# Kernel optimization log

Hardware: AMD Instinct MI355X
Metric: run time of the kernel (lower is better)

## Reference

```python
import jax, jax.numpy as jnp
import numpy as np

B, D = 128, 16384
EPS = 0.05
MAX_DEPTH = 5
D_MAX = 1000.0


def setup_inputs() -> dict:
    key = jax.random.key(0)
    k1, k2 = jax.random.split(key)
    theta = jax.random.normal(k1, (B, D), dtype=jnp.float32)
    prec = jax.random.uniform(k2, (D,), dtype=jnp.float32)
    return {"theta": theta, "prec": prec}


def _energy(theta, prec):
    # per-chain potential energy U(theta): [B]
    return 0.5 * jnp.einsum('bd,d,bd->b', theta, prec, theta)


def _grad_energy(theta, prec):
    # mirrors torch autograd.grad(energy.sum(), theta)
    return jax.grad(lambda th: _energy(th, prec).sum())(theta)


def _bdot(a, b):
    return jnp.einsum('bd,bd->b', a, b)


def _leapfrog(theta, r, prec, eps):
    gU = _grad_energy(theta, prec)
    r = r - 0.5 * eps * gU
    theta = theta + eps * r
    e = _energy(theta, prec)
    gU = _grad_energy(theta, prec)
    r = r - 0.5 * eps * gU
    return theta, r, e


def _buildtree(theta, r, u, eps_dir, j, key, prec):
    # returns (theta_near, r_near, theta_far, r_far, theta_prop, n, s)
    if j == 0:
        th, rp, e = _leapfrog(theta, r, prec, eps_dir)
        H = e + 0.5 * _bdot(rp, rp)
        n_p = (u <= jnp.exp(-H)).astype(jnp.int32)
        s_p = (jnp.log(u) - D_MAX < -H).astype(jnp.int32)
        return th, rp, th, rp, th, n_p, s_p
    k1, k2, k3 = jax.random.split(key, 3)
    th_n, r_n, th_f, r_f, th_p, n_p, s_p = _buildtree(theta, r, u, eps_dir, j - 1, k1, prec)
    _, _, th_f2, r_f2, th_pp, n_pp, s_pp = _buildtree(th_f, r_f, u, eps_dir, j - 1, k2, prec)
    # accept proposal from second subtree with prob n'' / (n' + n''), masked by s'
    denom = jnp.maximum(n_p + n_pp, 1).astype(jnp.float32)
    flag = (jax.random.uniform(k3, n_p.shape) < n_pp.astype(jnp.float32) / denom) & (s_p >= 1)
    th_p = jnp.where(flag[:, None], th_pp, th_p)
    # u-turn check; v*(far - near) == theta_plus - theta_minus
    v = jnp.sign(eps_dir)
    d = th_f2 - th_n
    s_new = (s_p * s_pp
             * ((v * _bdot(d, r_n)) >= 0.0).astype(jnp.int32)
             * ((v * _bdot(d, r_f2)) >= 0.0).astype(jnp.int32))
    n_new = n_p + jnp.where(s_p >= 1, n_pp, 0)
    return th_n, r_n, th_f2, r_f2, th_p, n_new, s_new


def _sample_trajectory(theta0, prec, key):
    kr, ku, key = jax.random.split(key, 3)
    r0 = jax.random.normal(kr, theta0.shape, theta0.dtype)
    H0 = _energy(theta0, prec) + 0.5 * _bdot(r0, r0)
    u = jax.random.uniform(ku, H0.shape, theta0.dtype) * jnp.exp(-H0)
    theta_r = theta0
    theta_f = theta0
    r_r = r0
    r_f = r0
    theta_m = theta0
    n = jnp.ones((theta0.shape[0],), jnp.int32)
    s = jnp.ones((theta0.shape[0],), jnp.int32)
    for j in range(MAX_DEPTH):  # tree doubling, bounded depth (jit-friendly)
        key, kv, kt, ka = jax.random.split(key, 4)
        v = jnp.where(jax.random.normal(kv, ()) >= 0.0, 1.0, -1.0)
        neg = v < 0.0
        st_th = jnp.where(neg, theta_r, theta_f)
        st_r = jnp.where(neg, r_r, r_f)
        _, _, th_far, r_far, th_p, n_p, s_p = _buildtree(st_th, st_r, u, v * EPS, j, kt, prec)
        theta_r = jnp.where(neg, th_far, theta_r)
        r_r = jnp.where(neg, r_far, r_r)
        theta_f = jnp.where(neg, theta_f, th_far)
        r_f = jnp.where(neg, r_f, r_far)
        acc = jax.random.uniform(ka, n.shape) < jnp.minimum(
            n_p.astype(jnp.float32) / n.astype(jnp.float32), 1.0)
        acc = acc & (s >= 1) & (s_p >= 1)
        theta_m = jnp.where(acc[:, None], th_p, theta_m)
        n = n + jnp.where(s >= 1, n_p, 0)
        d = theta_f - theta_r
        s = (s * s_p
             * (_bdot(d, r_r) >= 0.0).astype(jnp.int32)
             * (_bdot(d, r_f) >= 0.0).astype(jnp.int32))
    return theta_m


def reference(theta, prec):
    return _sample_trajectory(theta, prec, jax.random.key(42))
```

## Files before the change

### kernel.cpp

```cpp
#include <hip/hip_runtime.h>
#include <cstdint>
#include <cstring>


#define PARTITIONABLE 1

constexpr int NCHAIN = 128;
constexpr int NDIM   = 16384;
constexpr int VD     = 4;
constexpr int TPB    = 256;
constexpr int WGPC   = NDIM / (TPB * VD);
constexpr int NW     = NDIM / (64 * VD);
constexpr int NSLOT  = 62;
constexpr int NNODE  = 26;
constexpr float EPS  = 0.05f;

static_assert(NDIM % (TPB * VD) == 0, "tiling");

__host__ __device__ static inline void tf2(uint32_t k0, uint32_t k1,
                                           uint32_t x0, uint32_t x1,
                                           uint32_t& o0, uint32_t& o1) {
  const uint32_t ks2 = k0 ^ k1 ^ 0x1BD11BDAu;
  x0 += k0; x1 += k1;
#define TF_R(r) { x0 += x1; x1 = (x1 << (r)) | (x1 >> (32 - (r))); x1 ^= x0; }
  TF_R(13) TF_R(15) TF_R(26) TF_R(6)
  x0 += k1;  x1 += ks2 + 1u;
  TF_R(17) TF_R(29) TF_R(16) TF_R(24)
  x0 += ks2; x1 += k0 + 2u;
  TF_R(13) TF_R(15) TF_R(26) TF_R(6)
  x0 += k0;  x1 += k1 + 3u;
  TF_R(17) TF_R(29) TF_R(16) TF_R(24)
  x0 += k1;  x1 += ks2 + 4u;
  TF_R(13) TF_R(15) TF_R(26) TF_R(6)
  x0 += ks2; x1 += k0 + 5u;
#undef TF_R
  o0 = x0; o1 = x1;
}

__device__ static inline float u01(uint32_t bits) {
  return __uint_as_float((bits >> 9) | 0x3f800000u) - 1.0f;
}

__device__ static inline float erfinv32(float x) {
  float w = -log1pf(-x * x);
  float p;
  if (w < 5.0f) {
    w -= 2.5f;
    p = 2.81022636e-08f;
    p = fmaf(p, w, 3.43273939e-07f);
    p = fmaf(p, w, -3.5233877e-06f);
    p = fmaf(p, w, -4.39150654e-06f);
    p = fmaf(p, w, 0.00021858087f);
    p = fmaf(p, w, -0.00125372503f);
    p = fmaf(p, w, -0.00417768164f);
    p = fmaf(p, w, 0.246640727f);
    p = fmaf(p, w, 1.50140941f);
  } else {
    w = sqrtf(w) - 3.0f;
    p = -0.000200214257f;
    p = fmaf(p, w, 0.000100950558f);
    p = fmaf(p, w, 0.00134934322f);
    p = fmaf(p, w, -0.00367342844f);
    p = fmaf(p, w, 0.00573950773f);
    p = fmaf(p, w, -0.0076224613f);
    p = fmaf(p, w, 0.00943887047f);
    p = fmaf(p, w, 1.00167406f);
    p = fmaf(p, w, 2.83297682f);
  }
  return p * x;
}

__device__ static inline float norm_from_bits(uint32_t bits) {
  const float lo = __uint_as_float(0xBF7FFFFFu);
  float u = fmaxf(lo, fmaf(u01(bits), 2.0f, lo));
  return __uint_as_float(0x3FB504F3u) * erfinv32(u);
}

__device__ static inline float r0_elem(uint32_t k0, uint32_t k1, uint32_t i) {
#if PARTITIONABLE
  uint32_t a, c; tf2(k0, k1, 0u, i, a, c);
  return norm_from_bits(a ^ c);
#else
  const uint32_t H = (uint32_t)(NCHAIN * NDIM / 2);
  uint32_t a, c;
  if (i < H) { tf2(k0, k1, i, i + H, a, c); return norm_from_bits(a); }
  else       { tf2(k0, k1, i - H, i, a, c); return norm_from_bits(c); }
#endif
}

__device__ static inline float unif_chain(uint32_t k0, uint32_t k1, int b) {
#if PARTITIONABLE
  uint32_t a, c; tf2(k0, k1, 0u, (uint32_t)b, a, c);
  return u01(a ^ c);
#else
  uint32_t a, c;
  if (b < 64) { tf2(k0, k1, (uint32_t)b, (uint32_t)(b + 64), a, c); return u01(a); }
  else        { tf2(k0, k1, (uint32_t)(b - 64), (uint32_t)b, a, c); return u01(c); }
#endif
}

#define DPP_ADD(x, ctrl, rm)                                                   \
  (x) += __int_as_float(__builtin_amdgcn_update_dpp(                           \
      0, __float_as_int(x), (ctrl), (rm), 0xf, true));

__device__ static inline float wave_sum63(float x) {
  DPP_ADD(x, 0x111, 0xf)
  DPP_ADD(x, 0x112, 0xf)
  DPP_ADD(x, 0x114, 0xf)
  DPP_ADD(x, 0x118, 0xf)
  DPP_ADD(x, 0x142, 0xa)
  DPP_ADD(x, 0x143, 0xc)
  return x;
}

struct TrajParams { int v[5]; };
struct K2Params {
  uint32_t nk0[NNODE], nk1[NNODE];
  uint32_t ak0[5], ak1[5];
  int v[5];
};

struct St {
  float tha[VD], ra[VD], tho[VD], ro[VD], pc[VD];
  float nt[5][VD], nr[5][VD];
};

template <int J, int I>
__device__ __forceinline__ void leaf_body(St& st, const float e, const float he,
                                          float* __restrict__ partials,
                                          const int chain, const int wv,
                                          const int lane, int& slot) {
#pragma unroll
  for (int d = 0; d < VD; ++d) {
    st.ra[d]  = fmaf(-he, st.pc[d] * st.tha[d], st.ra[d]);
    st.tha[d] = fmaf(e, st.ra[d], st.tha[d]);
    st.ra[d]  = fmaf(-he, st.pc[d] * st.tha[d], st.ra[d]);
  }
  constexpr int P = __builtin_popcount((unsigned)I);
#pragma unroll
  for (int d = 0; d < VD; ++d) { st.nt[P][d] = st.tha[d]; st.nr[P][d] = st.ra[d]; }
  constexpr int M = __builtin_ctz(~(unsigned)I);
#pragma unroll
  for (int k = 0; k < M; ++k) {
    const int s1 = P - 1 - k;
    float d1 = 0.f, d2 = 0.f;
#pragma unroll
    for (int d = 0; d < VD; ++d) {
      float dd = st.tha[d] - st.nt[s1][d];
      d1 = fmaf(dd, st.nr[s1][d], d1);
      d2 = fmaf(dd, st.ra[d], d2);
    }
    d1 = wave_sum63(d1);
    d2 = wave_sum63(d2);
    if (lane == 63) {
      partials[((size_t)(slot    ) * NCHAIN + chain) * NW + wv] = d1;
      partials[((size_t)(slot + 1) * NCHAIN + chain) * NW + wv] = d2;
    }
    slot += 2;
  }
}

template <int J, int I>
__device__ __forceinline__ void run_level(St& st, const float e, const float he,
                                          float* __restrict__ partials,
                                          const int chain, const int wv,
                                          const int lane, int& slot) {
  leaf_body<J, I>(st, e, he, partials, chain, wv, lane, slot);
  if constexpr (I + 1 < (1 << J))
    run_level<J, I + 1>(st, e, he, partials, chain, wv, lane, slot);
}

__launch_bounds__(TPB, 2)
__global__ void k_traj0(const float* __restrict__ th0g, const float* __restrict__ precg,
                        uint32_t kr0, uint32_t kr1,
                        float* __restrict__ partials, TrajParams P) {
  const int tid     = threadIdx.x;
  const int chain   = blockIdx.x / WGPC;
  const int sblk    = blockIdx.x % WGPC;
  const int dimBase = sblk * (TPB * VD) + tid * VD;
  const int lane    = tid & 63;
  const int wv      = sblk * (TPB / 64) + (tid >> 6);
  const uint32_t flat = (uint32_t)chain * NDIM + dimBase;

  St st;
  {
    const float4 t = *reinterpret_cast<const float4*>(th0g + (size_t)chain * NDIM + dimBase);
    const float4 p = *reinterpret_cast<const float4*>(precg + dimBase);
    st.tha[0]=t.x; st.tha[1]=t.y; st.tha[2]=t.z; st.tha[3]=t.w;
    st.pc [0]=p.x; st.pc [1]=p.y; st.pc [2]=p.z; st.pc [3]=p.w;
  }
#pragma unroll
  for (int d = 0; d < VD; ++d) st.ra[d] = r0_elem(kr0, kr1, flat + (uint32_t)d);
#pragma unroll
  for (int d = 0; d < VD; ++d) { st.tho[d] = st.tha[d]; st.ro[d] = st.ra[d]; }

  int slot = 0;
  bool cur_fwd = true;

#define LEVEL(J)                                                               \
  {                                                                            \
    const bool fwd = P.v[J] > 0;                                               \
    if (fwd != cur_fwd) {                                                      \
      _Pragma("unroll")                                                        \
      for (int d = 0; d < VD; ++d) {                                           \
        float t;                                                               \
        t = st.tha[d]; st.tha[d] = st.tho[d]; st.tho[d] = t;                   \
        t = st.ra[d];  st.ra[d]  = st.ro[d];  st.ro[d]  = t;                   \
      }                                                                        \
    }                                                                          \
    cur_fwd = fwd;                                                             \
    const float e  = fwd ? EPS : -EPS;                                         \
    const float he = 0.5f * e;                                                 \
    run_level<J, 0>(st, e, he, partials, chain, wv, lane, slot);               \
    float p1 = 0.f, p2 = 0.f;                                                  \
    _Pragma("unroll")                                                          \
    for (int d = 0; d < VD; ++d) {                                             \
      float dd = st.tha[d] - st.tho[d];                                        \
      p1 = fmaf(dd, st.ra[d], p1);                                             \
      p2 = fmaf(dd, st.ro[d], p2);                                             \
    }                                                                          \
    p1 = wave_sum63(p1);                                                       \
    p2 = wave_sum63(p2);                                                       \
    if (lane == 63) {                                                          \
      partials[((size_t)(slot    ) * NCHAIN + chain) * NW + wv] = p1;          \
      partials[((size_t)(slot + 1) * NCHAIN + chain) * NW + wv] = p2;          \
    }                                                                          \
    slot += 2;                                                                 \
  }

  LEVEL(0) LEVEL(1) LEVEL(2) LEVEL(3) LEVEL(4)
#undef LEVEL
}

__global__ void k_red(const float* __restrict__ partials, float* __restrict__ dots) {
  int gid  = blockIdx.x * blockDim.x + threadIdx.x;
  int w    = gid >> 6;
  int lane = gid & 63;
  if (w >= NSLOT * NCHAIN) return;
  float v = partials[(size_t)w * NW + lane];
  v = wave_sum63(v);
  if (lane == 63) dots[w] = v;
}

__global__ void k_logic(const float* __restrict__ dots, int* __restrict__ selg,
                        K2Params P) {
  int b = threadIdx.x;
  if (b >= NCHAIN) return;
  int n = 1, s = 1, sel = -1;
  int slot = 0, nodeidx = 0, g = 0;
  int st_n[6], st_s[6], st_p[6];
  for (int j = 0; j < 5; ++j) {
    float vj = (P.v[j] > 0) ? 1.0f : -1.0f;
    int sp = 0;
    int NL = 1 << j;
    for (int i = 0; i < NL; ++i) {
      st_n[sp] = 1; st_s[sp] = 1; st_p[sp] = g; sp++; g++;
      int m = __builtin_ctz(~(unsigned)i);
      for (int k = 0; k < m; ++k) {
        int n1 = st_n[sp-2], s1 = st_s[sp-2], p1i = st_p[sp-2];
        int n2 = st_n[sp-1], s2 = st_s[sp-1], p2i = st_p[sp-1];
        float d1 = dots[(size_t)(slot    ) * NCHAIN + b];
        float d2 = dots[(size_t)(slot + 1) * NCHAIN + b];
        slot += 2;
        float uu = unif_chain(P.nk0[nodeidx], P.nk1[nodeidx], b);
        nodeidx++;
        int   dn    = n1 + n2; if (dn < 1) dn = 1;
        bool  flag  = (uu < (float)n2 / (float)dn) && (s1 >= 1);
        int   pm    = flag ? p2i : p1i;
        int   sm    = (s1 != 0 && s2 != 0 &&
                       (vj * d1 >= 0.0f) && (vj * d2 >= 0.0f)) ? 1 : 0;
        int   nm    = n1 + ((s1 >= 1) ? n2 : 0);
        st_n[sp-2] = nm; st_s[sp-2] = sm; st_p[sp-2] = pm;
        sp--;
      }
    }
    int n_p = st_n[0], s_p = st_s[0], th_p = st_p[0];
    float q1 = dots[(size_t)(slot    ) * NCHAIN + b];
    float q2 = dots[(size_t)(slot + 1) * NCHAIN + b];
    slot += 2;
    float dm1, dm2;
    if (P.v[j] > 0) { dm1 = q2;  dm2 = q1; }
    else            { dm1 = -q1; dm2 = -q2; }
    float au = unif_chain(P.ak0[j], P.ak1[j], b);
    float ratio = fminf((float)n_p / (float)n, 1.0f);
    bool acc = (au < ratio) && (s >= 1) && (s_p >= 1);
    if (acc) sel = th_p;
    n = n + ((s >= 1) ? n_p : 0);
    s = (s != 0 && s_p != 0 && (dm1 >= 0.0f) && (dm2 >= 0.0f)) ? 1 : 0;
  }
  selg[b] = sel;
}

__launch_bounds__(TPB, 2)
__global__ void k_gather(const float* __restrict__ th0g, const float* __restrict__ precg,
                         uint32_t kr0, uint32_t kr1,
                         const int* __restrict__ selg, float* __restrict__ outg,
                         TrajParams P) {
  const int chain   = blockIdx.x / WGPC;
  const int sblk    = blockIdx.x % WGPC;
  const int dimBase = sblk * (TPB * VD) + threadIdx.x * VD;
  const uint32_t flat = (uint32_t)chain * NDIM + dimBase;
  const int sel = selg[chain];

  float tha[VD], ra[VD], tho[VD], ro[VD], pc[VD], outv[VD];
  {
    const float4 t = *reinterpret_cast<const float4*>(th0g + (size_t)chain * NDIM + dimBase);
    const float4 p = *reinterpret_cast<const float4*>(precg + dimBase);
    tha[0]=t.x; tha[1]=t.y; tha[2]=t.z; tha[3]=t.w;
    pc [0]=p.x; pc [1]=p.y; pc [2]=p.z; pc [3]=p.w;
  }
#pragma unroll
  for (int d = 0; d < VD; ++d) outv[d] = tha[d];
  if (sel >= 0) {
#pragma unroll
    for (int d = 0; d < VD; ++d) ra[d] = r0_elem(kr0, kr1, flat + (uint32_t)d);
#pragma unroll
    for (int d = 0; d < VD; ++d) { tho[d] = tha[d]; ro[d] = ra[d]; }
    int g = 0;
    bool cur_fwd = true;
    bool done = false;
    for (int j = 0; j < 5 && !done; ++j) {
      const bool fwd = P.v[j] > 0;
      if (fwd != cur_fwd) {
#pragma unroll
        for (int d = 0; d < VD; ++d) {
          float t;
          t = tha[d]; tha[d] = tho[d]; tho[d] = t;
          t = ra[d];  ra[d]  = ro[d];  ro[d]  = t;
        }
      }
      cur_fwd = fwd;
      const float e  = fwd ? EPS : -EPS;
      const float he = 0.5f * e;
      const int NL = 1 << j;
      for (int i = 0; i < NL; ++i) {
#pragma unroll
        for (int d = 0; d < VD; ++d) {
          ra[d]  = fmaf(-he, pc[d] * tha[d], ra[d]);
          tha[d] = fmaf(e, ra[d], tha[d]);
          ra[d]  = fmaf(-he, pc[d] * tha[d], ra[d]);
        }
        if (g == sel) {
#pragma unroll
          for (int d = 0; d < VD; ++d) outv[d] = tha[d];
          done = true;
          break;
        }
        g++;
      }
    }
  }
  float4 o; o.x = outv[0]; o.y = outv[1]; o.z = outv[2]; o.w = outv[3];
  *reinterpret_cast<float4*>(outg + (size_t)chain * NDIM + dimBase) = o;
}

static inline float host_bits_to_f(uint32_t fb) { float f; std::memcpy(&f, &fb, 4); return f; }

static void host_split(uint32_t k0, uint32_t k1, int nsub, uint32_t* o0, uint32_t* o1) {
#if PARTITIONABLE
  for (int i = 0; i < nsub; ++i) tf2(k0, k1, 0u, (uint32_t)i, o0[i], o1[i]);
#else
  uint32_t A[8], C[8], flat[16];
  for (int i = 0; i < nsub; ++i) tf2(k0, k1, (uint32_t)i, (uint32_t)(nsub + i), A[i], C[i]);
  for (int i = 0; i < nsub; ++i) { flat[i] = A[i]; flat[nsub + i] = C[i]; }
  for (int j = 0; j < nsub; ++j) { o0[j] = flat[2*j]; o1[j] = flat[2*j + 1]; }
#endif
}

static int host_vsign(uint32_t k0, uint32_t k1) {
  uint32_t a, c; tf2(k0, k1, 0u, 0u, a, c);
#if PARTITIONABLE
  uint32_t bits = a ^ c;
#else
  uint32_t bits = a;
#endif
  float f  = host_bits_to_f((bits >> 9) | 0x3f800000u) - 1.0f;
  float lo = host_bits_to_f(0xBF7FFFFFu);
  float u  = f * 2.0f + lo;
  return (u >= 0.0f) ? 1 : -1;
}

static void gen_nodes(uint32_t k0, uint32_t k1, int j,
                      uint32_t* nk0, uint32_t* nk1, int& idx) {
  if (j == 0) return;
  uint32_t o0[3], o1[3];
  host_split(k0, k1, 3, o0, o1);
  gen_nodes(o0[0], o1[0], j - 1, nk0, nk1, idx);
  gen_nodes(o0[1], o1[1], j - 1, nk0, nk1, idx);
  nk0[idx] = o0[2]; nk1[idx] = o1[2]; idx++;
}

extern "C" void kernel_launch(void* const* d_in, const int* in_sizes, int n_in,
                              void* d_out, int out_size, void* d_ws, size_t ws_size,
                              hipStream_t stream) {
  const float* th0  = (const float*)d_in[0];
  const float* prec = (const float*)d_in[1];
  float* out = (float*)d_out;

  float* partials = (float*)d_ws;
  float* dots     = partials + (size_t)NSLOT * NCHAIN * NW;
  int*   sel      = (int*)(dots + (size_t)NSLOT * NCHAIN);

  uint32_t key0 = 0u, key1 = 42u;
  uint32_t s0[4], s1[4];
  host_split(key0, key1, 3, s0, s1);
  const uint32_t kr0 = s0[0], kr1 = s1[0];
  key0 = s0[2]; key1 = s1[2];

  K2Params P2; TrajParams PT;
  int idx = 0;
  for (int j = 0; j < 5; ++j) {
    host_split(key0, key1, 4, s0, s1);
    key0 = s0[0]; key1 = s1[0];
    int v = host_vsign(s0[1], s1[1]);
    P2.v[j] = v; PT.v[j] = v;
    gen_nodes(s0[2], s1[2], j, P2.nk0, P2.nk1, idx);
    P2.ak0[j] = s0[3]; P2.ak1[j] = s1[3];
  }

  k_traj0<<<dim3(NCHAIN * WGPC), dim3(TPB), 0, stream>>>(
      th0, prec, kr0, kr1, partials, PT);
  k_red<<<dim3((NSLOT * NCHAIN * 64) / TPB), dim3(TPB), 0, stream>>>(partials, dots);
  k_logic<<<dim3(1), dim3(NCHAIN), 0, stream>>>(dots, sel, P2);
  k_gather<<<dim3(NCHAIN * WGPC), dim3(TPB), 0, stream>>>(
      th0, prec, kr0, kr1, sel, out, PT);
}
```

Measured before the change: 123.6 us.

## Fuse trajectory, reduction, NUTS logic and gather into one last-block kernel

```diff
diff --git a/kernel.cpp b/kernel.cpp
--- a/kernel.cpp
+++ b/kernel.cpp
@@ -113,8 +113,7 @@
   return x;
 }
 
-struct TrajParams { int v[5]; };
-struct K2Params {
+struct Params {
   uint32_t nk0[NNODE], nk1[NNODE];
   uint32_t ak0[5], ak1[5];
   int v[5];
@@ -170,10 +169,73 @@
     run_level<J, I + 1>(st, e, he, partials, chain, wv, lane, slot);
 }
 
+struct SM {
+  int n, s, sel, slot, nodeidx, g;
+  int st_n[5], st_s[5], st_p[5];
+};
+
+template <int J, int I>
+__device__ __forceinline__ void sm_leaf(SM& m, const float* dots_s,
+                                        const float* unifs_s, const float vj) {
+  constexpr int P = __builtin_popcount((unsigned)I);
+  m.st_n[P] = 1; m.st_s[P] = 1; m.st_p[P] = m.g; m.g++;
+  constexpr int M = __builtin_ctz(~(unsigned)I);
+#pragma unroll
+  for (int k = 0; k < M; ++k) {
+    const int t = P - k;
+    int n1 = m.st_n[t-1], s1 = m.st_s[t-1], p1 = m.st_p[t-1];
+    int n2 = m.st_n[t],   s2 = m.st_s[t],   p2 = m.st_p[t];
+    float d1 = dots_s[m.slot], d2 = dots_s[m.slot + 1];
+    m.slot += 2;
+    float uu = unifs_s[m.nodeidx]; m.nodeidx++;
+    int dn = n1 + n2; if (dn < 1) dn = 1;
+    bool fl = (uu < (float)n2 / (float)dn) && (s1 >= 1);
+    m.st_p[t-1] = fl ? p2 : p1;
+    m.st_s[t-1] = (s1 != 0 && s2 != 0 &&
+                   (vj * d1 >= 0.0f) && (vj * d2 >= 0.0f)) ? 1 : 0;
+    m.st_n[t-1] = n1 + ((s1 >= 1) ? n2 : 0);
+  }
+}
+
+template <int J, int I>
+__device__ __forceinline__ void sm_level(SM& m, const float* dots_s,
+                                         const float* unifs_s, const float vj) {
+  sm_leaf<J, I>(m, dots_s, unifs_s, vj);
+  if constexpr (I + 1 < (1 << J))
+    sm_level<J, I + 1>(m, dots_s, unifs_s, vj);
+}
+
+template <int J>
+__device__ __forceinline__ void sm_close(SM& m, const float* dots_s,
+                                         const float* unifs_s, const int vj) {
+  int n_p = m.st_n[0], s_p = m.st_s[0], th_p = m.st_p[0];
+  float q1 = dots_s[m.slot], q2 = dots_s[m.slot + 1];
+  m.slot += 2;
+  float dm1, dm2;
+  if (vj > 0) { dm1 = q2;  dm2 = q1; }
+  else        { dm1 = -q1; dm2 = -q2; }
+  float au = unifs_s[NNODE + J];
+  float ratio = fminf((float)n_p / (float)m.n, 1.0f);
+  bool acc = (au < ratio) && (m.s >= 1) && (s_p >= 1);
+  if (acc) m.sel = th_p;
+  m.n = m.n + ((m.s >= 1) ? n_p : 0);
+  m.s = (m.s != 0 && s_p != 0 && (dm1 >= 0.0f) && (dm2 >= 0.0f)) ? 1 : 0;
+}
+
+__global__ void k_zero(unsigned* __restrict__ done) {
+  if (threadIdx.x < NCHAIN) done[threadIdx.x] = 0u;
+}
+
 __launch_bounds__(TPB, 2)
-__global__ void k_traj0(const float* __restrict__ th0g, const float* __restrict__ precg,
-                        uint32_t kr0, uint32_t kr1,
-                        float* __restrict__ partials, TrajParams P) {
+__global__ void k_main(const float* __restrict__ th0g, const float* __restrict__ precg,
+                       uint32_t kr0, uint32_t kr1,
+                       float* __restrict__ partials, float* __restrict__ r0save,
+                       unsigned* __restrict__ done, float* __restrict__ outg,
+                       Params P) {
+  __shared__ float dots_s[NSLOT];
+  __shared__ float unifs_s[NNODE + 5];
+  __shared__ int   sh_last;
+
   const int tid     = threadIdx.x;
   const int chain   = blockIdx.x / WGPC;
   const int sblk    = blockIdx.x % WGPC;
@@ -182,176 +244,149 @@
   const int wv      = sblk * (TPB / 64) + (tid >> 6);
   const uint32_t flat = (uint32_t)chain * NDIM + dimBase;
 
-  St st;
   {
-    const float4 t = *reinterpret_cast<const float4*>(th0g + (size_t)chain * NDIM + dimBase);
-    const float4 p = *reinterpret_cast<const float4*>(precg + dimBase);
-    st.tha[0]=t.x; st.tha[1]=t.y; st.tha[2]=t.z; st.tha[3]=t.w;
-    st.pc [0]=p.x; st.pc [1]=p.y; st.pc [2]=p.z; st.pc [3]=p.w;
-  }
-#pragma unroll
-  for (int d = 0; d < VD; ++d) st.ra[d] = r0_elem(kr0, kr1, flat + (uint32_t)d);
-#pragma unroll
-  for (int d = 0; d < VD; ++d) { st.tho[d] = st.tha[d]; st.ro[d] = st.ra[d]; }
-
-  int slot = 0;
-  bool cur_fwd = true;
+    St st;
+    {
+      const float4 t = *reinterpret_cast<const float4*>(th0g + (size_t)chain * NDIM + dimBase);
+      const float4 p = *reinterpret_cast<const float4*>(precg + dimBase);
+      st.tha[0]=t.x; st.tha[1]=t.y; st.tha[2]=t.z; st.tha[3]=t.w;
+      st.pc [0]=p.x; st.pc [1]=p.y; st.pc [2]=p.z; st.pc [3]=p.w;
+    }
+#pragma unroll
+    for (int d = 0; d < VD; ++d) st.ra[d] = r0_elem(kr0, kr1, flat + (uint32_t)d);
+    {
+      float4 r; r.x = st.ra[0]; r.y = st.ra[1]; r.z = st.ra[2]; r.w = st.ra[3];
+      *reinterpret_cast<float4*>(r0save + (size_t)flat) = r;
+    }
+#pragma unroll
+    for (int d = 0; d < VD; ++d) { st.tho[d] = st.tha[d]; st.ro[d] = st.ra[d]; }
+
+    int slot = 0;
+    bool cur_fwd = true;
 
 #define LEVEL(J)                                                               \
-  {                                                                            \
-    const bool fwd = P.v[J] > 0;                                               \
-    if (fwd != cur_fwd) {                                                      \
+    {                                                                          \
+      const bool fwd = P.v[J] > 0;                                             \
+      if (fwd != cur_fwd) {                                                    \
+        _Pragma("unroll")                                                      \
+        for (int d = 0; d < VD; ++d) {                                         \
+          float t;                                                             \
+          t = st.tha[d]; st.tha[d] = st.tho[d]; st.tho[d] = t;                 \
+          t = st.ra[d];  st.ra[d]  = st.ro[d];  st.ro[d]  = t;                 \
+        }                                                                      \
+      }                                                                        \
+      cur_fwd = fwd;                                                           \
+      const float e  = fwd ? EPS : -EPS;                                       \
+      const float he = 0.5f * e;                                               \
+      run_level<J, 0>(st, e, he, partials, chain, wv, lane, slot);             \
+      float p1 = 0.f, p2 = 0.f;                                                \
       _Pragma("unroll")                                                        \
       for (int d = 0; d < VD; ++d) {                                           \
-        float t;                                                               \
-        t = st.tha[d]; st.tha[d] = st.tho[d]; st.tho[d] = t;                   \
-        t = st.ra[d];  st.ra[d]  = st.ro[d];  st.ro[d]  = t;                   \
+        float dd = st.tha[d] - st.tho[d];                                      \
+        p1 = fmaf(dd, st.ra[d], p1);                                           \
+        p2 = fmaf(dd, st.ro[d], p2);                                           \
       }                                                                        \
-    }                                                                          \
-    cur_fwd = fwd;                                                             \
-    const float e  = fwd ? EPS : -EPS;                                         \
-    const float he = 0.5f * e;                                                 \
-    run_level<J, 0>(st, e, he, partials, chain, wv, lane, slot);               \
-    float p1 = 0.f, p2 = 0.f;                                                  \
-    _Pragma("unroll")                                                          \
-    for (int d = 0; d < VD; ++d) {                                             \
-      float dd = st.tha[d] - st.tho[d];                                        \
-      p1 = fmaf(dd, st.ra[d], p1);                                             \
-      p2 = fmaf(dd, st.ro[d], p2);                                             \
-    }                                                                          \
-    p1 = wave_sum63(p1);                                                       \
-    p2 = wave_sum63(p2);                                                       \
-    if (lane == 63) {                                                          \
-      partials[((size_t)(slot    ) * NCHAIN + chain) * NW + wv] = p1;          \
-      partials[((size_t)(slot + 1) * NCHAIN + chain) * NW + wv] = p2;          \
-    }                                                                          \
-    slot += 2;                                                                 \
-  }
-
-  LEVEL(0) LEVEL(1) LEVEL(2) LEVEL(3) LEVEL(4)
+      p1 = wave_sum63(p1);                                                     \
+      p2 = wave_sum63(p2);                                                     \
+      if (lane == 63) {                                                        \
+        partials[((size_t)(slot    ) * NCHAIN + chain) * NW + wv] = p1;        \
+        partials[((size_t)(slot + 1) * NCHAIN + chain) * NW + wv] = p2;        \
+      }                                                                        \
+      slot += 2;                                                               \
+    }
+
+    LEVEL(0) LEVEL(1) LEVEL(2) LEVEL(3) LEVEL(4)
 #undef LEVEL
-}
-
-__global__ void k_red(const float* __restrict__ partials, float* __restrict__ dots) {
-  int gid  = blockIdx.x * blockDim.x + threadIdx.x;
-  int w    = gid >> 6;
-  int lane = gid & 63;
-  if (w >= NSLOT * NCHAIN) return;
-  float v = partials[(size_t)w * NW + lane];
-  v = wave_sum63(v);
-  if (lane == 63) dots[w] = v;
-}
-
-__global__ void k_logic(const float* __restrict__ dots, int* __restrict__ selg,
-                        K2Params P) {
-  int b = threadIdx.x;
-  if (b >= NCHAIN) return;
-  int n = 1, s = 1, sel = -1;
-  int slot = 0, nodeidx = 0, g = 0;
-  int st_n[6], st_s[6], st_p[6];
-  for (int j = 0; j < 5; ++j) {
-    float vj = (P.v[j] > 0) ? 1.0f : -1.0f;
-    int sp = 0;
-    int NL = 1 << j;
-    for (int i = 0; i < NL; ++i) {
-      st_n[sp] = 1; st_s[sp] = 1; st_p[sp] = g; sp++; g++;
-      int m = __builtin_ctz(~(unsigned)i);
-      for (int k = 0; k < m; ++k) {
-        int n1 = st_n[sp-2], s1 = st_s[sp-2], p1i = st_p[sp-2];
-        int n2 = st_n[sp-1], s2 = st_s[sp-1], p2i = st_p[sp-1];
-        float d1 = dots[(size_t)(slot    ) * NCHAIN + b];
-        float d2 = dots[(size_t)(slot + 1) * NCHAIN + b];
-        slot += 2;
-        float uu = unif_chain(P.nk0[nodeidx], P.nk1[nodeidx], b);
-        nodeidx++;
-        int   dn    = n1 + n2; if (dn < 1) dn = 1;
-        bool  flag  = (uu < (float)n2 / (float)dn) && (s1 >= 1);
-        int   pm    = flag ? p2i : p1i;
-        int   sm    = (s1 != 0 && s2 != 0 &&
-                       (vj * d1 >= 0.0f) && (vj * d2 >= 0.0f)) ? 1 : 0;
-        int   nm    = n1 + ((s1 >= 1) ? n2 : 0);
-        st_n[sp-2] = nm; st_s[sp-2] = sm; st_p[sp-2] = pm;
-        sp--;
-      }
-    }
-    int n_p = st_n[0], s_p = st_s[0], th_p = st_p[0];
-    float q1 = dots[(size_t)(slot    ) * NCHAIN + b];
-    float q2 = dots[(size_t)(slot + 1) * NCHAIN + b];
-    slot += 2;
-    float dm1, dm2;
-    if (P.v[j] > 0) { dm1 = q2;  dm2 = q1; }
-    else            { dm1 = -q1; dm2 = -q2; }
-    float au = unif_chain(P.ak0[j], P.ak1[j], b);
-    float ratio = fminf((float)n_p / (float)n, 1.0f);
-    bool acc = (au < ratio) && (s >= 1) && (s_p >= 1);
-    if (acc) sel = th_p;
-    n = n + ((s >= 1) ? n_p : 0);
-    s = (s != 0 && s_p != 0 && (dm1 >= 0.0f) && (dm2 >= 0.0f)) ? 1 : 0;
-  }
-  selg[b] = sel;
-}
-
-__launch_bounds__(TPB, 2)
-__global__ void k_gather(const float* __restrict__ th0g, const float* __restrict__ precg,
-                         uint32_t kr0, uint32_t kr1,
-                         const int* __restrict__ selg, float* __restrict__ outg,
-                         TrajParams P) {
-  const int chain   = blockIdx.x / WGPC;
-  const int sblk    = blockIdx.x % WGPC;
-  const int dimBase = sblk * (TPB * VD) + threadIdx.x * VD;
-  const uint32_t flat = (uint32_t)chain * NDIM + dimBase;
-  const int sel = selg[chain];
-
-  float tha[VD], ra[VD], tho[VD], ro[VD], pc[VD], outv[VD];
-  {
-    const float4 t = *reinterpret_cast<const float4*>(th0g + (size_t)chain * NDIM + dimBase);
-    const float4 p = *reinterpret_cast<const float4*>(precg + dimBase);
-    tha[0]=t.x; tha[1]=t.y; tha[2]=t.z; tha[3]=t.w;
-    pc [0]=p.x; pc [1]=p.y; pc [2]=p.z; pc [3]=p.w;
-  }
-#pragma unroll
-  for (int d = 0; d < VD; ++d) outv[d] = tha[d];
-  if (sel >= 0) {
-#pragma unroll
-    for (int d = 0; d < VD; ++d) ra[d] = r0_elem(kr0, kr1, flat + (uint32_t)d);
-#pragma unroll
-    for (int d = 0; d < VD; ++d) { tho[d] = tha[d]; ro[d] = ra[d]; }
-    int g = 0;
-    bool cur_fwd = true;
-    bool done = false;
-    for (int j = 0; j < 5 && !done; ++j) {
-      const bool fwd = P.v[j] > 0;
-      if (fwd != cur_fwd) {
-#pragma unroll
-        for (int d = 0; d < VD; ++d) {
-          float t;
-          t = tha[d]; tha[d] = tho[d]; tho[d] = t;
-          t = ra[d];  ra[d]  = ro[d];  ro[d]  = t;
+  }
+
+  __threadfence();
+  __syncthreads();
+  if (tid == 0) {
+    unsigned old = __hip_atomic_fetch_add(&done[chain], 1u,
+                                          __ATOMIC_ACQ_REL, __HIP_MEMORY_SCOPE_AGENT);
+    sh_last = (old == (unsigned)(WGPC - 1));
+  }
+  __syncthreads();
+  if (!sh_last) return;
+  __threadfence();
+
+  if (tid < NNODE) unifs_s[tid] = unif_chain(P.nk0[tid], P.nk1[tid], chain);
+  else if (tid < NNODE + 5)
+    unifs_s[tid] = unif_chain(P.ak0[tid - NNODE], P.ak1[tid - NNODE], chain);
+
+  for (int s = (tid >> 6); s < NSLOT; s += TPB / 64) {
+    float v = partials[((size_t)s * NCHAIN + chain) * NW + lane];
+    v = wave_sum63(v);
+    if (lane == 63) dots_s[s] = v;
+  }
+  __syncthreads();
+
+  SM m;
+  m.n = 1; m.s = 1; m.sel = -1; m.slot = 0; m.nodeidx = 0; m.g = 0;
+#define SLEVEL(J)                                                              \
+  {                                                                            \
+    const float vj = (P.v[J] > 0) ? 1.0f : -1.0f;                              \
+    sm_level<J, 0>(m, dots_s, unifs_s, vj);                                    \
+    sm_close<J>(m, dots_s, unifs_s, P.v[J]);                                   \
+  }
+  SLEVEL(0) SLEVEL(1) SLEVEL(2) SLEVEL(3) SLEVEL(4)
+#undef SLEVEL
+  const int sel = m.sel;
+
+  for (int grp = 0; grp < WGPC; ++grp) {
+    const int db = grp * (TPB * VD) + tid * VD;
+    const size_t off = (size_t)chain * NDIM + db;
+    float tha[VD], ra[VD], tho[VD], ro[VD], pc[VD], outv[VD];
+    {
+      const float4 t = *reinterpret_cast<const float4*>(th0g + off);
+      tha[0]=t.x; tha[1]=t.y; tha[2]=t.z; tha[3]=t.w;
+    }
+#pragma unroll
+    for (int d = 0; d < VD; ++d) outv[d] = tha[d];
+    if (sel >= 0) {
+      const float4 p = *reinterpret_cast<const float4*>(precg + db);
+      const float4 r = *reinterpret_cast<const float4*>(r0save + off);
+      pc[0]=p.x; pc[1]=p.y; pc[2]=p.z; pc[3]=p.w;
+      ra[0]=r.x; ra[1]=r.y; ra[2]=r.z; ra[3]=r.w;
+#pragma unroll
+      for (int d = 0; d < VD; ++d) { tho[d] = tha[d]; ro[d] = ra[d]; }
+      int g = 0;
+      bool cur_fwd = true;
+      bool fin = false;
+      for (int j = 0; j < 5 && !fin; ++j) {
+        const bool fwd = P.v[j] > 0;
+        if (fwd != cur_fwd) {
+#pragma unroll
+          for (int d = 0; d < VD; ++d) {
+            float t;
+            t = tha[d]; tha[d] = tho[d]; tho[d] = t;
+            t = ra[d];  ra[d]  = ro[d];  ro[d]  = t;
+          }
+        }
+        cur_fwd = fwd;
+        const float e  = fwd ? EPS : -EPS;
+        const float he = 0.5f * e;
+        const int NL = 1 << j;
+        for (int i = 0; i < NL; ++i) {
+#pragma unroll
+          for (int d = 0; d < VD; ++d) {
+            ra[d]  = fmaf(-he, pc[d] * tha[d], ra[d]);
+            tha[d] = fmaf(e, ra[d], tha[d]);
+            ra[d]  = fmaf(-he, pc[d] * tha[d], ra[d]);
+          }
+          if (g == sel) {
+#pragma unroll
+            for (int d = 0; d < VD; ++d) outv[d] = tha[d];
+            fin = true;
+            break;
+          }
+          g++;
         }
       }
-      cur_fwd = fwd;
-      const float e  = fwd ? EPS : -EPS;
-      const float he = 0.5f * e;
-      const int NL = 1 << j;
-      for (int i = 0; i < NL; ++i) {
-#pragma unroll
-        for (int d = 0; d < VD; ++d) {
-          ra[d]  = fmaf(-he, pc[d] * tha[d], ra[d]);
-          tha[d] = fmaf(e, ra[d], tha[d]);
-          ra[d]  = fmaf(-he, pc[d] * tha[d], ra[d]);
-        }
-        if (g == sel) {
-#pragma unroll
-          for (int d = 0; d < VD; ++d) outv[d] = tha[d];
-          done = true;
-          break;
-        }
-        g++;
-      }
-    }
-  }
-  float4 o; o.x = outv[0]; o.y = outv[1]; o.z = outv[2]; o.w = outv[3];
-  *reinterpret_cast<float4*>(outg + (size_t)chain * NDIM + dimBase) = o;
+    }
+    float4 o; o.x = outv[0]; o.y = outv[1]; o.z = outv[2]; o.w = outv[3];
+    *reinterpret_cast<float4*>(outg + off) = o;
+  }
 }
 
 static inline float host_bits_to_f(uint32_t fb) { float f; std::memcpy(&f, &fb, 4); return f; }
@@ -397,9 +432,9 @@
   const float* prec = (const float*)d_in[1];
   float* out = (float*)d_out;
 
-  float* partials = (float*)d_ws;
-  float* dots     = partials + (size_t)NSLOT * NCHAIN * NW;
-  int*   sel      = (int*)(dots + (size_t)NSLOT * NCHAIN);
+  float*    partials = (float*)d_ws;
+  float*    r0save   = partials + (size_t)NSLOT * NCHAIN * NW;
+  unsigned* done     = (unsigned*)(r0save + (size_t)NCHAIN * NDIM);
 
   uint32_t key0 = 0u, key1 = 42u;
   uint32_t s0[4], s1[4];
@@ -407,21 +442,17 @@
   const uint32_t kr0 = s0[0], kr1 = s1[0];
   key0 = s0[2]; key1 = s1[2];
 
-  K2Params P2; TrajParams PT;
+  Params P;
   int idx = 0;
   for (int j = 0; j < 5; ++j) {
     host_split(key0, key1, 4, s0, s1);
     key0 = s0[0]; key1 = s1[0];
-    int v = host_vsign(s0[1], s1[1]);
-    P2.v[j] = v; PT.v[j] = v;
-    gen_nodes(s0[2], s1[2], j, P2.nk0, P2.nk1, idx);
-    P2.ak0[j] = s0[3]; P2.ak1[j] = s1[3];
-  }
-
-  k_traj0<<<dim3(NCHAIN * WGPC), dim3(TPB), 0, stream>>>(
-      th0, prec, kr0, kr1, partials, PT);
-  k_red<<<dim3((NSLOT * NCHAIN * 64) / TPB), dim3(TPB), 0, stream>>>(partials, dots);
-  k_logic<<<dim3(1), dim3(NCHAIN), 0, stream>>>(dots, sel, P2);
-  k_gather<<<dim3(NCHAIN * WGPC), dim3(TPB), 0, stream>>>(
-      th0, prec, kr0, kr1, sel, out, PT);
-}
+    P.v[j] = host_vsign(s0[1], s1[1]);
+    gen_nodes(s0[2], s1[2], j, P.nk0, P.nk1, idx);
+    P.ak0[j] = s0[3]; P.ak1[j] = s1[3];
+  }
+
+  k_zero<<<dim3(1), dim3(NCHAIN), 0, stream>>>(done);
+  k_main<<<dim3(NCHAIN * WGPC), dim3(TPB), 0, stream>>>(
+      th0, prec, kr0, kr1, partials, r0save, done, out, P);
+}
```

After: 488.5 us. 3.95x slower.
